# Optimization experiments

Hardware: AMD Instinct MI355X
Metric: run time of the kernel (lower is better)

The kernel has to match this reference:

```python
import math
import jax, jax.numpy as jnp
import numpy as np

K_VALUE = 2
CAPACITY_FACTOR_TRAIN = 1.25
MIN_CAPACITY = 4


def _get_capacity(s, e):
    capacity = math.floor(K_VALUE * CAPACITY_FACTOR_TRAIN * s / e)
    capacity += capacity % 2
    capacity = max(capacity, MIN_CAPACITY)
    return capacity


def setup_inputs() -> dict:
    key = jax.random.key(0)
    inputs = jax.random.normal(key, (8192, 8), dtype=jnp.float32)
    return {"inputs": inputs}


def reference(inputs):
    s, e = inputs.shape  # tokens, experts (static)
    capacity = _get_capacity(s, e)

    logits = jax.nn.softmax(inputs, axis=-1)  # [s, e]

    # top-1 / top-2 expert selection via masked argmax (matches torch argmax semantics)
    top1_idx = jnp.argmax(logits, axis=-1)  # [s]
    mask1 = jax.nn.one_hot(top1_idx, e, dtype=jnp.int32)  # [s, e]
    logits_except1 = jnp.where(mask1.astype(bool), -jnp.inf, logits)
    top2_idx = jnp.argmax(logits_except1, axis=-1)
    mask2 = jax.nn.one_hot(top2_idx, e, dtype=jnp.int32)

    # position-in-expert rank via exclusive cumsum over tokens (moe_cumsum = cumsum - 1)
    rank1 = jnp.cumsum(mask1, axis=0) - 1  # [s, e]
    rank2 = jnp.cumsum(mask2, axis=0) - 1 + jnp.sum(mask1, axis=0, keepdims=True)

    # drop tokens beyond capacity
    mask1 = mask1 * (rank1 < capacity).astype(jnp.int32)
    mask2 = mask2 * (rank2 < capacity).astype(jnp.int32)

    # scalar slot index per token
    rank1 = jnp.sum(mask1 * rank1, axis=-1)  # [s]
    rank2 = jnp.sum(mask2 * rank2, axis=-1)

    weight1 = mask1.astype(inputs.dtype) * logits  # [s, e]
    weight2 = mask2.astype(inputs.dtype) * logits

    rank1_sc = jax.nn.one_hot(rank1, capacity, dtype=inputs.dtype)  # [s, c]
    rank2_sc = jax.nn.one_hot(rank2, capacity, dtype=inputs.dtype)

    # combine weights: [s, e, c]
    cb_weight = weight1[:, :, None] * rank1_sc[:, None, :] + weight2[:, :, None] * rank2_sc[:, None, :]
    sec_mask = cb_weight.astype(bool)
    return cb_weight, sec_mask
```

## Files before the change

### kernel.cpp

```cpp
#include <hip/hip_runtime.h>
#include <hip/hip_bf16.h>
#include <stdint.h>


#define ST 1024
#define ROUNDS 8

__global__ __launch_bounds__(ST) void router_kernel(
    const float* __restrict__ in, float4* __restrict__ table, int s, int cap) {
  __shared__ int wc1[ST / 64][8], wc2[ST / 64][8];
  __shared__ int base1[8], base2[8];
  const int tid = threadIdx.x;
  const int lane = tid & 63;
  const int wave = tid >> 6;
  const unsigned long long lt = (lane == 0) ? 0ULL : (~0ULL >> (64 - lane));

  if (tid < 8) { base1[tid] = 0; base2[tid] = 0; }
  __syncthreads();

  int e1a[ROUNDS], e2a[ROUNDS], r1a[ROUNDS], r2a[ROUNDS];
  float w1a[ROUNDS], w2a[ROUNDS];

#pragma unroll
  for (int k = 0; k < ROUNDS; ++k) {
    const int t = k * ST + tid;
    int e1 = -1, e2 = -1;
    float w1 = 0.f, w2 = 0.f;
    if (t < s) {
      const float4* p = reinterpret_cast<const float4*>(in + (size_t)t * 8);
      const float4 a = p[0], b = p[1];
      float v[8] = {a.x, a.y, a.z, a.w, b.x, b.y, b.z, b.w};
      float m = v[0];
#pragma unroll
      for (int i = 1; i < 8; ++i) m = fmaxf(m, v[i]);
      float ex[8], sum = 0.f;
#pragma unroll
      for (int i = 0; i < 8; ++i) { ex[i] = expf(v[i] - m); sum += ex[i]; }
      const float inv = 1.0f / sum;
      e1 = 0; float b1 = v[0];
#pragma unroll
      for (int i = 1; i < 8; ++i) { if (v[i] > b1) { b1 = v[i]; e1 = i; } }
      float b2 = -1e38f; e2 = 0;
#pragma unroll
      for (int i = 0; i < 8; ++i) {
        if (i != e1 && v[i] > b2) { b2 = v[i]; e2 = i; }
      }
      w1 = ex[e1] * inv;
      w2 = ex[e2] * inv;
    }
    int lp1 = 0, lp2 = 0;
#pragma unroll
    for (int e = 0; e < 8; ++e) {
      const unsigned long long m1 = __ballot(e1 == e);
      const unsigned long long m2 = __ballot(e2 == e);
      if (lane == 0) { wc1[wave][e] = __popcll(m1); wc2[wave][e] = __popcll(m2); }
      if (e1 == e) lp1 = __popcll(m1 & lt);
      if (e2 == e) lp2 = __popcll(m2 & lt);
    }
    __syncthreads();
    int r1 = 0, r2 = 0;
    if (t < s) {
      int wp1 = 0, wp2 = 0;
      for (int w = 0; w < wave; ++w) { wp1 += wc1[w][e1]; wp2 += wc2[w][e2]; }
      r1 = base1[e1] + wp1 + lp1;
      r2 = base2[e2] + wp2 + lp2;
    }
    __syncthreads();
    if (tid < 8) {
      int a1 = 0, a2 = 0;
      for (int w = 0; w < ST / 64; ++w) { a1 += wc1[w][tid]; a2 += wc2[w][tid]; }
      base1[tid] += a1;
      base2[tid] += a2;
    }
    __syncthreads();
    e1a[k] = e1; e2a[k] = e2; r1a[k] = r1; r2a[k] = r2; w1a[k] = w1; w2a[k] = w2;
  }

#pragma unroll
  for (int k = 0; k < ROUNDS; ++k) {
    const int t = k * ST + tid;
    if (t >= s) continue;
    const int p1 = (r1a[k] < cap) ? e1a[k] * cap + r1a[k] : -1;
    const int rr2 = r2a[k] + base1[e2a[k]];
    const int p2 = (rr2 < cap) ? e2a[k] * cap + rr2 : -1;
    float4 rec;
    rec.x = __int_as_float(p1);
    rec.y = w1a[k];
    rec.z = __int_as_float(p2);
    rec.w = w2a[k];
    table[t] = rec;
  }
}

__global__ __launch_bounds__(256) void fill_kernel(float4* __restrict__ out,
                                                   unsigned n4) {
  unsigned i = blockIdx.x * 256u + threadIdx.x;
  const unsigned stride = gridDim.x * 256u;
  const float4 z = make_float4(0.f, 0.f, 0.f, 0.f);
  for (; i < n4; i += stride) out[i] = z;
}

__global__ __launch_bounds__(256) void scatter_kernel(
    const float4* __restrict__ table, float* __restrict__ out, int s, int row) {
  const int t = blockIdx.x * 256 + threadIdx.x;
  if (t >= s) return;
  const float4 rec = table[t];
  const int p1 = __float_as_int(rec.x);
  const int p2 = __float_as_int(rec.z);
  float* cb = out + (size_t)t * row;
  float* mk = cb + (size_t)s * row;
  if (p1 >= 0) { cb[p1] = rec.y; mk[p1] = (rec.y != 0.f) ? 1.f : 0.f; }
  if (p2 >= 0) { cb[p2] = rec.w; mk[p2] = (rec.w != 0.f) ? 1.f : 0.f; }
}

extern "C" void kernel_launch(void* const* d_in, const int* in_sizes, int n_in,
                              void* d_out, int out_size, void* d_ws, size_t ws_size,
                              hipStream_t stream) {
  const float* in = (const float*)d_in[0];
  const int E = 8;
  const int s = in_sizes[0] / E;
  int cap = (int)((5LL * s) / (2LL * E));
  cap += cap % 2;
  if (cap < 4) cap = 4;
  const int row = E * cap;

  float4* table = (float4*)d_ws;

  const unsigned n4 = (unsigned)((size_t)out_size / 4);
  fill_kernel<<<2048, 256, 0, stream>>>((float4*)d_out, n4);
  router_kernel<<<1, ST, 0, stream>>>(in, table, s, cap);
  scatter_kernel<<<(s + 255) / 256, 256, 0, stream>>>(table, (float*)d_out, s, row);
}
```

Before: 1.381 ms.

## Fuse zero-fill and scatter into one pass writing final output values

Replaces the separate zero-fill and sparse-scatter kernels with a single grid-stride kernel. Each float4 of the combine-weight and mask planes is computed from the token's routing record and written once. This drops one full pass of scattered writes and one kernel launch, and removes the write-after-write dependency between fill and scatter. In exchange, every output element now needs a table lookup and an integer divide by the row width, specialised at compile time for the common row size.

Measured after the change: 1.322 ms. 4.3% less time.

```diff
diff --git a/kernel.cpp b/kernel.cpp
--- a/kernel.cpp
+++ b/kernel.cpp
@@ -92,25 +92,32 @@
   }
 }
 
-__global__ __launch_bounds__(256) void fill_kernel(float4* __restrict__ out,
-                                                   unsigned n4) {
+template <unsigned CROW4>
+__global__ __launch_bounds__(256) void fused_fill_scatter(
+    const float4* __restrict__ table, float4* __restrict__ out,
+    unsigned plane4, unsigned row4_rt) {
+  const unsigned row4 = CROW4 ? CROW4 : row4_rt;
   unsigned i = blockIdx.x * 256u + threadIdx.x;
   const unsigned stride = gridDim.x * 256u;
-  const float4 z = make_float4(0.f, 0.f, 0.f, 0.f);
-  for (; i < n4; i += stride) out[i] = z;
-}
-
-__global__ __launch_bounds__(256) void scatter_kernel(
-    const float4* __restrict__ table, float* __restrict__ out, int s, int row) {
-  const int t = blockIdx.x * 256 + threadIdx.x;
-  if (t >= s) return;
-  const float4 rec = table[t];
-  const int p1 = __float_as_int(rec.x);
-  const int p2 = __float_as_int(rec.z);
-  float* cb = out + (size_t)t * row;
-  float* mk = cb + (size_t)s * row;
-  if (p1 >= 0) { cb[p1] = rec.y; mk[p1] = (rec.y != 0.f) ? 1.f : 0.f; }
-  if (p2 >= 0) { cb[p2] = rec.w; mk[p2] = (rec.w != 0.f) ? 1.f : 0.f; }
+  const unsigned total = plane4 * 2u;
+  for (; i < total; i += stride) {
+    const bool maskplane = (i >= plane4);
+    const unsigned j = maskplane ? i - plane4 : i;
+    const unsigned t = j / row4;
+    const int c0 = (int)((j - t * row4) * 4u);
+    const float4 rec = table[t];
+    const int p1 = __float_as_int(rec.x);
+    const int p2 = __float_as_int(rec.z);
+    float4 v = make_float4(0.f, 0.f, 0.f, 0.f);
+    float* vp = reinterpret_cast<float*>(&v);
+#pragma unroll
+    for (int c = 0; c < 4; ++c) {
+      const int pos = c0 + c;
+      if (pos == p1) vp[c] = maskplane ? ((rec.y != 0.f) ? 1.f : 0.f) : rec.y;
+      if (pos == p2) vp[c] = maskplane ? ((rec.w != 0.f) ? 1.f : 0.f) : rec.w;
+    }
+    out[i] = v;
+  }
 }
 
 extern "C" void kernel_launch(void* const* d_in, const int* in_sizes, int n_in,
@@ -123,11 +130,17 @@
   cap += cap % 2;
   if (cap < 4) cap = 4;
   const int row = E * cap;
+  const unsigned row4 = row / 4;
+  const unsigned plane4 = (unsigned)s * row4;
 
   float4* table = (float4*)d_ws;
 
-  const unsigned n4 = (unsigned)((size_t)out_size / 4);
-  fill_kernel<<<2048, 256, 0, stream>>>((float4*)d_out, n4);
   router_kernel<<<1, ST, 0, stream>>>(in, table, s, cap);
-  scatter_kernel<<<(s + 255) / 256, 256, 0, stream>>>(table, (float*)d_out, s, row);
+  if (row4 == 5120u) {
+    fused_fill_scatter<5120u><<<2048, 256, 0, stream>>>(
+        table, (float4*)d_out, plane4, row4);
+  } else {
+    fused_fill_scatter<0u><<<2048, 256, 0, stream>>>(
+        table, (float4*)d_out, plane4, row4);
+  }
 }
```
